# Performance work log

Measured on AMD Instinct MI355X. Metric: run time of the kernel, lower is better.

Reference implementation:

```python
import jax, jax.numpy as jnp
import numpy as np

N = 100000        # total nodes across the batch of graphs
E = 1600000       # directed edges (avg degree 16)
B = 64            # number of graphs
IN_C = 4
HID = 128


def gcn_conv(x, W, b, src, dst, n):
    """PyG GCNConv: add self-loops, symmetric deg normalization, scatter-add."""
    h = x @ W                                   # [n, out]
    loop = jnp.arange(n)
    s = jnp.concatenate([src, loop])            # [E+n] sources (with self-loops)
    d = jnp.concatenate([dst, loop])            # [E+n] targets
    deg = jax.ops.segment_sum(jnp.ones_like(s, dtype=h.dtype), d, num_segments=n)
    dinv = jnp.where(deg > 0, jax.lax.rsqrt(deg), 0.0)
    norm = dinv[s] * dinv[d]                    # [E+n]
    out = jax.ops.segment_sum(h[s] * norm[:, None], d, num_segments=n)
    return out + b


def setup_inputs() -> dict:
    key = jax.random.key(0)
    k1, k2, k3, k4, k5, k6, k7 = jax.random.split(key, 7)
    x = jax.random.normal(k1, (N, IN_C), dtype=jnp.float32)
    edge_index = jax.random.randint(k2, (2, E), 0, N, dtype=jnp.int64)
    batch = jnp.sort(jax.random.randint(k3, (N,), 0, B, dtype=jnp.int64))
    W1 = jax.random.normal(k4, (IN_C, HID), dtype=jnp.float32) / np.sqrt(IN_C)
    b1 = jnp.zeros((HID,), dtype=jnp.float32)
    W2 = jax.random.normal(k5, (HID, HID), dtype=jnp.float32) / np.sqrt(HID)
    b2 = jnp.zeros((HID,), dtype=jnp.float32)
    return {"x": x, "edge_index": edge_index, "batch": batch,
            "W1": W1, "b1": b1, "W2": W2, "b2": b2}


def reference(x, edge_index, batch, W1, b1, W2, b2):
    src, dst = edge_index[0], edge_index[1]
    n = x.shape[0]
    h = jax.nn.relu(gcn_conv(x, W1, b1, src, dst, n))
    h = jax.nn.relu(gcn_conv(h, W2, b2, src, dst, n))
    # global_mean_pool: scatter-mean by graph id
    s = jax.ops.segment_sum(h, batch, num_segments=B)                       # [B, HID]
    cnt = jax.ops.segment_sum(jnp.ones((n,), h.dtype), batch, num_segments=B)
    return s / jnp.maximum(cnt, 1.0)[:, None]
```

## Files before the change

### kernel.cpp

```cpp
#include <hip/hip_runtime.h>

#define TPB 256
#define HID 128
#define IN_C 4
#define SLOT_C 32
#define NB 512
#define EPT 8
#define ECAP 4096
#define OVF_CAP 131072

typedef __attribute__((ext_vector_type(8))) short bf16x8;
typedef __attribute__((ext_vector_type(4))) float f32x4;

union FragU { uint4 u; bf16x8 b; };

__device__ __forceinline__ unsigned f2bf(float f) {
    unsigned u = __float_as_uint(f);
    return (u + 0x7fffu + ((u >> 16) & 1u)) >> 16;
}
__device__ __forceinline__ float bf_lo(unsigned u) { return __uint_as_float(u << 16); }
__device__ __forceinline__ float bf_hi(unsigned u) { return __uint_as_float(u & 0xffff0000u); }

__global__ void k_prep(float* out, int n, int outsz,
                       const float* __restrict__ W2, unsigned short* w2f,
                       const int* __restrict__ batch, float* rcnt, int bg,
                       int* ovf_cnt, int* pcur) {
    int nbA = (n + TPB - 1) / TPB;
    int b = blockIdx.x;
    if (b < nbA) {
        int i = b * TPB + threadIdx.x;
        if (i < outsz) out[i] = 0.0f;
    } else if (b < nbA + 64) {
        int i = (b - nbA) * TPB + threadIdx.x;
        if (i < HID * HID) {
            int j = i & 7, frag = i >> 3;
            int lane = frag & 63, blk = frag >> 6;
            int kk = blk >> 3, nt = blk & 7;
            int quad = lane >> 4, nloc = lane & 15;
            int k = kk * 32 + quad * 8 + j;
            int c = nt * 16 + nloc;
            w2f[i] = (unsigned short)f2bf(W2[k * HID + c]);
        }
    } else {
        int g = threadIdx.x;
        if (g == 0) *ovf_cnt = 0;
        for (int z = g; z < NB; z += TPB) pcur[z] = 0;
        if (g < bg) {
            int lo0 = 0, hi0 = n;
            while (lo0 < hi0) { int m = (lo0 + hi0) >> 1; if (batch[m] < g) lo0 = m + 1; else hi0 = m; }
            int lo1 = lo0, hi1 = n;
            while (lo1 < hi1) { int m = (lo1 + hi1) >> 1; if (batch[m] < g + 1) lo1 = m + 1; else hi1 = m; }
            int c = lo1 - lo0;
            rcnt[g] = 1.0f / (float)(c > 1 ? c : 1);
        }
    }
}

__global__ __launch_bounds__(256) void k_part(
        const int* __restrict__ src, const int* __restrict__ dst,
        unsigned* elist, int* pcur, int e, int n) {
    __shared__ int lcnt[2][NB];
    __shared__ int lbase[NB];
    int t = threadIdx.x;
    int c = (t >> 5) & 1;
    for (int z = t; z < NB; z += 256) { lcnt[0][z] = 0; lcnt[1][z] = 0; }
    __syncthreads();

    int base_i = blockIdx.x * (256 * EPT);
    unsigned u[EPT]; int pr[EPT];
#pragma unroll
    for (int k = 0; k < EPT; k++) {
        int i = base_i + k * 256 + t;
        if (i < e) {
            int s = src[i];
            int d = dst[i];
            int p = (int)(((long long)d * NB) / n);
            int nlo = (int)(((long long)p * n + NB - 1) / NB);
            int r = atomicAdd(&lcnt[c][p], 1);
            pr[k] = p | (r << 9);
            u[k] = (unsigned)s | ((unsigned)(d - nlo) << 17);
        } else {
            pr[k] = -1;
        }
    }
    __syncthreads();

    for (int z = t; z < NB; z += 256) {
        int tot = lcnt[0][z] + lcnt[1][z];
        lbase[z] = tot ? atomicAdd(&pcur[z], tot) : 0;
    }
    __syncthreads();

#pragma unroll
    for (int k = 0; k < EPT; k++) {
        if (pr[k] >= 0) {
            int p = pr[k] & (NB - 1);
            int r = pr[k] >> 9;
            int idx = lbase[p] + (c ? lcnt[0][p] : 0) + r;
            if (idx < ECAP)
                elist[(size_t)p * ECAP + idx] = u[k];
        }
    }
}

__global__ __launch_bounds__(256) void k_build(
        const unsigned* __restrict__ elist, const int* __restrict__ pcur,
        int* cursor, float* dinv, int* slots, int* ovf, int* ovf_cnt, int n) {
    __shared__ int lcur[512];
    int p = blockIdx.x;
    int t = threadIdx.x;
    int nlo = (int)(((long long)p * n + NB - 1) / NB);
    int nhi = (int)(((long long)(p + 1) * n + NB - 1) / NB);
    int nn = nhi - nlo;
    for (int z = t; z < nn; z += 256) lcur[z] = 0;
    __syncthreads();

    int ne = pcur[p];
    if (ne > ECAP) ne = ECAP;
    for (int j = t; j < ne; j += 256) {
        unsigned u = elist[(size_t)p * ECAP + j];
        int s = (int)(u & 0x1FFFFu);
        int dloc = (int)(u >> 17);
        int pos = atomicAdd(&lcur[dloc], 1);
        if (pos < SLOT_C) {
            slots[(nlo + dloc) * SLOT_C + pos] = s;
        } else {
            int o = atomicAdd(ovf_cnt, 1);
            if (o < OVF_CAP) {
                ovf[2 * o] = s;
                ovf[2 * o + 1] = nlo + dloc;
            }
        }
    }
    __syncthreads();
    for (int z = t; z < nn; z += 256) {
        int dg = lcur[z];
        cursor[nlo + z] = dg;
        dinv[nlo + z] = rsqrtf((float)dg + 1.0f);
    }
}

__global__ __launch_bounds__(256) void k_g1f1(
        const int* __restrict__ cursor, const int* __restrict__ slots,
        const int* __restrict__ ovf, const int* __restrict__ ovf_cnt,
        const float* __restrict__ dinv, const float* __restrict__ x,
        const float* __restrict__ W1, const float* __restrict__ b1,
        unsigned* f1p, int n) {
    __shared__ float xs[256 * 5];
    int t = threadIdx.x;
    int v0 = blockIdx.x * 256;

    int v = v0 + t;
    if (v < n) {
        float dv = dinv[v];
        const float4* x4 = (const float4*)x;
        float4 xv = x4[v];
        float sl = dv * dv;
        float4 A = make_float4(sl * xv.x, sl * xv.y, sl * xv.z, sl * xv.w);
        float4 B = make_float4(0.f, 0.f, 0.f, 0.f);
        float4 C = make_float4(0.f, 0.f, 0.f, 0.f);
        float4 D = make_float4(0.f, 0.f, 0.f, 0.f);
        int deg = cursor[v];
        int m = deg < SLOT_C ? deg : SLOT_C;
        const int* sb = slots + v * SLOT_C;
        int e = 0;
        for (; e + 4 <= m; e += 4) {
            int s0 = sb[e], s1 = sb[e + 1], s2 = sb[e + 2], s3 = sb[e + 3];
            float n0 = dinv[s0] * dv, n1 = dinv[s1] * dv;
            float n2 = dinv[s2] * dv, n3 = dinv[s3] * dv;
            float4 r0 = x4[s0], r1 = x4[s1], r2 = x4[s2], r3 = x4[s3];
            A.x = fmaf(n0, r0.x, A.x); A.y = fmaf(n0, r0.y, A.y);
            A.z = fmaf(n0, r0.z, A.z); A.w = fmaf(n0, r0.w, A.w);
            B.x = fmaf(n1, r1.x, B.x); B.y = fmaf(n1, r1.y, B.y);
            B.z = fmaf(n1, r1.z, B.z); B.w = fmaf(n1, r1.w, B.w);
            C.x = fmaf(n2, r2.x, C.x); C.y = fmaf(n2, r2.y, C.y);
            C.z = fmaf(n2, r2.z, C.z); C.w = fmaf(n2, r2.w, C.w);
            D.x = fmaf(n3, r3.x, D.x); D.y = fmaf(n3, r3.y, D.y);
            D.z = fmaf(n3, r3.z, D.z); D.w = fmaf(n3, r3.w, D.w);
        }
        for (; e < m; e++) {
            int s = sb[e];
            float nm = dinv[s] * dv;
            float4 r = x4[s];
            A.x = fmaf(nm, r.x, A.x); A.y = fmaf(nm, r.y, A.y);
            A.z = fmaf(nm, r.z, A.z); A.w = fmaf(nm, r.w, A.w);
        }
        if (deg > SLOT_C) {
            int oc = *ovf_cnt;
            for (int k = 0; k < oc; k++) {
                if (ovf[2 * k + 1] == v) {
                    int s = ovf[2 * k];
                    float nm = dinv[s] * dv;
                    float4 r = x4[s];
                    A.x = fmaf(nm, r.x, A.x); A.y = fmaf(nm, r.y, A.y);
                    A.z = fmaf(nm, r.z, A.z); A.w = fmaf(nm, r.w, A.w);
                }
            }
        }
        xs[t * 5 + 0] = (A.x + B.x) + (C.x + D.x);
        xs[t * 5 + 1] = (A.y + B.y) + (C.y + D.y);
        xs[t * 5 + 2] = (A.z + B.z) + (C.z + D.z);
        xs[t * 5 + 3] = (A.w + B.w) + (C.w + D.w);
    }
    __syncthreads();

    int cp = t & 63;
    int c0 = cp * 2, c1 = c0 + 1;
    float w00 = W1[c0],           w01 = W1[c1];
    float w10 = W1[HID + c0],     w11 = W1[HID + c1];
    float w20 = W1[2 * HID + c0], w21 = W1[2 * HID + c1];
    float w30 = W1[3 * HID + c0], w31 = W1[3 * HID + c1];
    float bb0 = b1[c0],           bb1 = b1[c1];
    int g = t >> 6;
    for (int iter = 0; iter < 64; iter++) {
        int node = iter * 4 + g;
        int vv = v0 + node;
        if (vv >= n) break;
        float x0 = xs[node * 5 + 0], x1 = xs[node * 5 + 1];
        float x2 = xs[node * 5 + 2], x3 = xs[node * 5 + 3];
        float s0 = fmaf(x0, w00, fmaf(x1, w10, fmaf(x2, w20, fmaf(x3, w30, bb0))));
        float s1 = fmaf(x0, w01, fmaf(x1, w11, fmaf(x2, w21, fmaf(x3, w31, bb1))));
        s0 = s0 > 0.0f ? s0 : 0.0f;
        s1 = s1 > 0.0f ? s1 : 0.0f;
        f1p[(size_t)vv * 64 + cp] = f2bf(s0) | (f2bf(s1) << 16);
    }
}

__global__ __launch_bounds__(128) void k_gather2(
        const int* __restrict__ cursor, const int* __restrict__ slots,
        const int* __restrict__ ovf, const int* __restrict__ ovf_cnt,
        const float* __restrict__ dinv, const unsigned* __restrict__ f1p,
        unsigned* acc2b, int n) {
    int wv = threadIdx.x >> 6;
    int ln = threadIdx.x & 63;
    int h  = ln >> 5;
    int q  = ln & 31;
    int v = blockIdx.x * 2 + wv;
    if (v >= n) return;
    float dv = dinv[v];
    const uint2* F = (const uint2*)f1p;

    uint2 us = F[(size_t)v * 32 + q];
    float sl = (h == 0) ? dv * dv : 0.0f;
    float A[4] = { sl * bf_lo(us.x), sl * bf_hi(us.x),
                   sl * bf_lo(us.y), sl * bf_hi(us.y) };
    float B[4] = {0.f, 0.f, 0.f, 0.f};
    float C[4] = {0.f, 0.f, 0.f, 0.f};
    float D[4] = {0.f, 0.f, 0.f, 0.f};

    int deg = cursor[v];
    int m = deg < SLOT_C ? deg : SLOT_C;
    const int* sb = slots + v * SLOT_C;
    int e = 0;
    for (; e + 8 <= m; e += 8) {
        int sA = sb[e + h];
        int sB = sb[e + 2 + h];
        int sC = sb[e + 4 + h];
        int sD = sb[e + 6 + h];
        float nA = dinv[sA] * dv, nB = dinv[sB] * dv;
        float nC = dinv[sC] * dv, nD = dinv[sD] * dv;
        uint2 uA = F[(size_t)sA * 32 + q];
        uint2 uB = F[(size_t)sB * 32 + q];
        uint2 uC = F[(size_t)sC * 32 + q];
        uint2 uD = F[(size_t)sD * 32 + q];
        A[0] = fmaf(nA, bf_lo(uA.x), A[0]); A[1] = fmaf(nA, bf_hi(uA.x), A[1]);
        A[2] = fmaf(nA, bf_lo(uA.y), A[2]); A[3] = fmaf(nA, bf_hi(uA.y), A[3]);
        B[0] = fmaf(nB, bf_lo(uB.x), B[0]); B[1] = fmaf(nB, bf_hi(uB.x), B[1]);
        B[2] = fmaf(nB, bf_lo(uB.y), B[2]); B[3] = fmaf(nB, bf_hi(uB.y), B[3]);
        C[0] = fmaf(nC, bf_lo(uC.x), C[0]); C[1] = fmaf(nC, bf_hi(uC.x), C[1]);
        C[2] = fmaf(nC, bf_lo(uC.y), C[2]); C[3] = fmaf(nC, bf_hi(uC.y), C[3]);
        D[0] = fmaf(nD, bf_lo(uD.x), D[0]); D[1] = fmaf(nD, bf_hi(uD.x), D[1]);
        D[2] = fmaf(nD, bf_lo(uD.y), D[2]); D[3] = fmaf(nD, bf_hi(uD.y), D[3]);
    }
    for (; e + 2 <= m; e += 2) {
        int s = sb[e + h];
        float nm = dinv[s] * dv;
        uint2 u = F[(size_t)s * 32 + q];
        A[0] = fmaf(nm, bf_lo(u.x), A[0]); A[1] = fmaf(nm, bf_hi(u.x), A[1]);
        A[2] = fmaf(nm, bf_lo(u.y), A[2]); A[3] = fmaf(nm, bf_hi(u.y), A[3]);
    }
    if (e < m) {
        int s = sb[e];
        float nm = (h == 0) ? dinv[s] * dv : 0.0f;
        uint2 u = F[(size_t)s * 32 + q];
        A[0] = fmaf(nm, bf_lo(u.x), A[0]); A[1] = fmaf(nm, bf_hi(u.x), A[1]);
        A[2] = fmaf(nm, bf_lo(u.y), A[2]); A[3] = fmaf(nm, bf_hi(u.y), A[3]);
    }
    if (deg > SLOT_C) {
        int oc = *ovf_cnt;
        for (int k = 0; k < oc; k++) {
            if (ovf[2 * k + 1] == v && h == 0) {
                int s = ovf[2 * k];
                float nm = dinv[s] * dv;
                uint2 u = F[(size_t)s * 32 + q];
                A[0] = fmaf(nm, bf_lo(u.x), A[0]); A[1] = fmaf(nm, bf_hi(u.x), A[1]);
                A[2] = fmaf(nm, bf_lo(u.y), A[2]); A[3] = fmaf(nm, bf_hi(u.y), A[3]);
            }
        }
    }

    float o0 = (A[0] + B[0]) + (C[0] + D[0]);
    float o1 = (A[1] + B[1]) + (C[1] + D[1]);
    float o2 = (A[2] + B[2]) + (C[2] + D[2]);
    float o3 = (A[3] + B[3]) + (C[3] + D[3]);
    o0 += __shfl_xor(o0, 32, 64);
    o1 += __shfl_xor(o1, 32, 64);
    o2 += __shfl_xor(o2, 32, 64);
    o3 += __shfl_xor(o3, 32, 64);
    if (h == 0) {
        uint2 w;
        w.x = f2bf(o0) | (f2bf(o1) << 16);
        w.y = f2bf(o2) | (f2bf(o3) << 16);
        ((uint2*)acc2b)[(size_t)v * 32 + q] = w;
    }
}

__global__ __launch_bounds__(256) void k_mm2_pool(
        const unsigned* __restrict__ acc2b, const unsigned short* __restrict__ w2f,
        const float* __restrict__ b2, const int* __restrict__ batch,
        const float* __restrict__ rcnt, float* out, int n) {
    __shared__ int bch[64];
    int t = threadIdx.x;
    int w = t >> 6, lane = t & 63;
    int quad = lane >> 4, nloc = lane & 15;
    int v0 = blockIdx.x * 64;
    if (t < 64) {
        int v = v0 + t;
        bch[t] = (v < n) ? batch[v] : -1;
    }
    __syncthreads();

    int va = v0 + w * 16 + nloc;
    if (va >= n) va = n - 1;

    const uint4* A4 = (const uint4*)acc2b;
    const uint4* B4 = (const uint4*)w2f;

    f32x4 acc[8];
#pragma unroll
    for (int nt = 0; nt < 8; nt++) acc[nt] = (f32x4){0.f, 0.f, 0.f, 0.f};

#pragma unroll
    for (int kk = 0; kk < 4; kk++) {
        FragU af;
        af.u = A4[(size_t)va * 16 + kk * 4 + quad];
#pragma unroll
        for (int nt = 0; nt < 8; nt++) {
            FragU bf;
            bf.u = B4[(kk * 8 + nt) * 64 + lane];
            acc[nt] = __builtin_amdgcn_mfma_f32_16x16x32_bf16(af.b, bf.b, acc[nt], 0, 0, 0);
        }
    }

    int b0 = bch[w * 16], b15 = bch[w * 16 + 15];
    if (b0 == b15 && b0 >= 0) {
        float rc = rcnt[b0];
#pragma unroll
        for (int nt = 0; nt < 8; nt++) {
            float bias = b2[nt * 16 + nloc];
            float s = 0.f;
#pragma unroll
            for (int reg = 0; reg < 4; reg++) {
                float f = acc[nt][reg] + bias;
                s += f > 0.f ? f : 0.f;
            }
            s += __shfl_xor(s, 16, 64);
            s += __shfl_xor(s, 32, 64);
            if (lane < 16) atomicAdd(&out[b0 * HID + nt * 16 + lane], s * rc);
        }
    } else {
#pragma unroll
        for (int nt = 0; nt < 8; nt++) {
            float bias = b2[nt * 16 + nloc];
            int cur = -1; float run = 0.f;
#pragma unroll
            for (int reg = 0; reg < 4; reg++) {
                int b = bch[w * 16 + quad * 4 + reg];
                if (b < 0) continue;
                float f = acc[nt][reg] + bias;
                f = f > 0.f ? f : 0.f;
                if (b != cur) {
                    if (cur >= 0) atomicAdd(&out[cur * HID + nt * 16 + nloc], run * rcnt[cur]);
                    run = 0.f; cur = b;
                }
                run += f;
            }
            if (cur >= 0) atomicAdd(&out[cur * HID + nt * 16 + nloc], run * rcnt[cur]);
        }
    }
}

extern "C" void kernel_launch(void* const* d_in, const int* in_sizes, int n_in,
                              void* d_out, int out_size, void* d_ws, size_t ws_size,
                              hipStream_t stream) {
    const float* x   = (const float*)d_in[0];
    const int* ei    = (const int*)d_in[1];
    const int* batch = (const int*)d_in[2];
    const float* W1  = (const float*)d_in[3];
    const float* b1  = (const float*)d_in[4];
    const float* W2  = (const float*)d_in[5];
    const float* b2  = (const float*)d_in[6];
    float* out = (float*)d_out;

    int n  = in_sizes[0] / IN_C;
    int e  = in_sizes[1] / 2;
    int bg = out_size / HID;
    const int* src = ei;
    const int* dst = ei + e;

    size_t off_b = 0;
    char* base = (char*)d_ws;
    auto carve = [&](size_t bytes) -> void* {
        void* p = base + off_b;
        off_b += (bytes + 255) & ~(size_t)255;
        return p;
    };
    int*            cursor  = (int*)carve((size_t)n * 4);
    int*            slots   = (int*)carve((size_t)n * SLOT_C * 4);
    int*            ovf     = (int*)carve((size_t)OVF_CAP * 2 * 4);
    int*            ovf_cnt = (int*)carve(256);
    int*            pcur    = (int*)carve((size_t)NB * 4);
    unsigned*       elist   = (unsigned*)carve((size_t)NB * ECAP * 4);
    float*          dinv    = (float*)carve((size_t)n * 4);
    unsigned*       f1p     = (unsigned*)carve((size_t)n * 64 * 4);
    unsigned*       acc2b   = (unsigned*)carve((size_t)n * 64 * 4);
    unsigned short* w2f     = (unsigned short*)carve((size_t)HID * HID * 2);
    float*          rcnt    = (float*)carve((size_t)bg * 4);
    (void)ws_size;

    int gN = (n + TPB - 1) / TPB;
    int gP = (e + 256 * EPT - 1) / (256 * EPT);

    k_prep<<<gN + 64 + 1, TPB, 0, stream>>>(out, n, out_size, W2, w2f,
                                            batch, rcnt, bg, ovf_cnt, pcur);
    k_part<<<gP, TPB, 0, stream>>>(src, dst, elist, pcur, e, n);
    k_build<<<NB, TPB, 0, stream>>>(elist, pcur, cursor, dinv, slots, ovf, ovf_cnt, n);
    k_g1f1<<<gN, TPB, 0, stream>>>(cursor, slots, ovf, ovf_cnt, dinv, x, W1, b1, f1p, n);
    k_gather2<<<(n + 1) / 2, 128, 0, stream>>>(cursor, slots, ovf, ovf_cnt, dinv, f1p, acc2b, n);
    k_mm2_pool<<<(n + 63) / 64, 256, 0, stream>>>(acc2b, w2f, b2, batch, rcnt, out, n);
}
```

Before: 242.3 us.

## Fuse layer-2 gather with MFMA matmul and pooling via shared memory

Merges the second-layer neighbor gather and the W2 matmul plus mean-pool into one kernel. Each 1024-thread block gathers 16 node rows into shared memory, then 8 waves each compute one 16-column MFMA tile and do the pooled atomics. This removes the bf16 intermediate buffer round-trip through global memory and one kernel launch. In exchange, half the waves sit idle during the matmul phase, every block pays a barrier, and each block now issues more atomics to the output.

```diff
diff --git a/kernel.cpp b/kernel.cpp
--- a/kernel.cpp
+++ b/kernel.cpp
@@ -226,158 +226,137 @@
     }
 }
 
-__global__ __launch_bounds__(128) void k_gather2(
+__global__ __launch_bounds__(1024, 8) void k_g2mm(
         const int* __restrict__ cursor, const int* __restrict__ slots,
         const int* __restrict__ ovf, const int* __restrict__ ovf_cnt,
         const float* __restrict__ dinv, const unsigned* __restrict__ f1p,
-        unsigned* acc2b, int n) {
-    int wv = threadIdx.x >> 6;
-    int ln = threadIdx.x & 63;
-    int h  = ln >> 5;
-    int q  = ln & 31;
-    int v = blockIdx.x * 2 + wv;
-    if (v >= n) return;
-    float dv = dinv[v];
+        const unsigned short* __restrict__ w2f, const float* __restrict__ b2,
+        const int* __restrict__ batch, const float* __restrict__ rcnt,
+        float* out, int n) {
+    __shared__ unsigned arow[16][68];
+    __shared__ int bch[16];
+    int t = threadIdx.x;
+    int w = t >> 6, ln = t & 63;
+    int v0 = blockIdx.x * 16;
+    if (t < 16) bch[t] = (v0 + t < n) ? batch[v0 + t] : -1;
+
+    int h = ln >> 5;
+    int q = ln & 31;
+    int v = v0 + w;
     const uint2* F = (const uint2*)f1p;
-
-    uint2 us = F[(size_t)v * 32 + q];
-    float sl = (h == 0) ? dv * dv : 0.0f;
-    float A[4] = { sl * bf_lo(us.x), sl * bf_hi(us.x),
-                   sl * bf_lo(us.y), sl * bf_hi(us.y) };
-    float B[4] = {0.f, 0.f, 0.f, 0.f};
-    float C[4] = {0.f, 0.f, 0.f, 0.f};
-    float D[4] = {0.f, 0.f, 0.f, 0.f};
-
-    int deg = cursor[v];
-    int m = deg < SLOT_C ? deg : SLOT_C;
-    const int* sb = slots + v * SLOT_C;
-    int e = 0;
-    for (; e + 8 <= m; e += 8) {
-        int sA = sb[e + h];
-        int sB = sb[e + 2 + h];
-        int sC = sb[e + 4 + h];
-        int sD = sb[e + 6 + h];
-        float nA = dinv[sA] * dv, nB = dinv[sB] * dv;
-        float nC = dinv[sC] * dv, nD = dinv[sD] * dv;
-        uint2 uA = F[(size_t)sA * 32 + q];
-        uint2 uB = F[(size_t)sB * 32 + q];
-        uint2 uC = F[(size_t)sC * 32 + q];
-        uint2 uD = F[(size_t)sD * 32 + q];
-        A[0] = fmaf(nA, bf_lo(uA.x), A[0]); A[1] = fmaf(nA, bf_hi(uA.x), A[1]);
-        A[2] = fmaf(nA, bf_lo(uA.y), A[2]); A[3] = fmaf(nA, bf_hi(uA.y), A[3]);
-        B[0] = fmaf(nB, bf_lo(uB.x), B[0]); B[1] = fmaf(nB, bf_hi(uB.x), B[1]);
-        B[2] = fmaf(nB, bf_lo(uB.y), B[2]); B[3] = fmaf(nB, bf_hi(uB.y), B[3]);
-        C[0] = fmaf(nC, bf_lo(uC.x), C[0]); C[1] = fmaf(nC, bf_hi(uC.x), C[1]);
-        C[2] = fmaf(nC, bf_lo(uC.y), C[2]); C[3] = fmaf(nC, bf_hi(uC.y), C[3]);
-        D[0] = fmaf(nD, bf_lo(uD.x), D[0]); D[1] = fmaf(nD, bf_hi(uD.x), D[1]);
-        D[2] = fmaf(nD, bf_lo(uD.y), D[2]); D[3] = fmaf(nD, bf_hi(uD.y), D[3]);
-    }
-    for (; e + 2 <= m; e += 2) {
-        int s = sb[e + h];
-        float nm = dinv[s] * dv;
-        uint2 u = F[(size_t)s * 32 + q];
-        A[0] = fmaf(nm, bf_lo(u.x), A[0]); A[1] = fmaf(nm, bf_hi(u.x), A[1]);
-        A[2] = fmaf(nm, bf_lo(u.y), A[2]); A[3] = fmaf(nm, bf_hi(u.y), A[3]);
-    }
-    if (e < m) {
-        int s = sb[e];
-        float nm = (h == 0) ? dinv[s] * dv : 0.0f;
-        uint2 u = F[(size_t)s * 32 + q];
-        A[0] = fmaf(nm, bf_lo(u.x), A[0]); A[1] = fmaf(nm, bf_hi(u.x), A[1]);
-        A[2] = fmaf(nm, bf_lo(u.y), A[2]); A[3] = fmaf(nm, bf_hi(u.y), A[3]);
-    }
-    if (deg > SLOT_C) {
-        int oc = *ovf_cnt;
-        for (int k = 0; k < oc; k++) {
-            if (ovf[2 * k + 1] == v && h == 0) {
-                int s = ovf[2 * k];
-                float nm = dinv[s] * dv;
-                uint2 u = F[(size_t)s * 32 + q];
-                A[0] = fmaf(nm, bf_lo(u.x), A[0]); A[1] = fmaf(nm, bf_hi(u.x), A[1]);
-                A[2] = fmaf(nm, bf_lo(u.y), A[2]); A[3] = fmaf(nm, bf_hi(u.y), A[3]);
+    if (v < n) {
+        float dv = dinv[v];
+        uint2 us = F[(size_t)v * 32 + q];
+        float sl = (h == 0) ? dv * dv : 0.0f;
+        float A[4] = { sl * bf_lo(us.x), sl * bf_hi(us.x),
+                       sl * bf_lo(us.y), sl * bf_hi(us.y) };
+        float B[4] = {0.f, 0.f, 0.f, 0.f};
+        float C[4] = {0.f, 0.f, 0.f, 0.f};
+        float D[4] = {0.f, 0.f, 0.f, 0.f};
+
+        int deg = cursor[v];
+        int m = deg < SLOT_C ? deg : SLOT_C;
+        const int* sb = slots + v * SLOT_C;
+        int e = 0;
+        for (; e + 8 <= m; e += 8) {
+            int sA = sb[e + h];
+            int sB = sb[e + 2 + h];
+            int sC = sb[e + 4 + h];
+            int sD = sb[e + 6 + h];
+            float nA = dinv[sA] * dv, nB = dinv[sB] * dv;
+            float nC = dinv[sC] * dv, nD = dinv[sD] * dv;
+            uint2 uA = F[(size_t)sA * 32 + q];
+            uint2 uB = F[(size_t)sB * 32 + q];
+            uint2 uC = F[(size_t)sC * 32 + q];
+            uint2 uD = F[(size_t)sD * 32 + q];
+            A[0] = fmaf(nA, bf_lo(uA.x), A[0]); A[1] = fmaf(nA, bf_hi(uA.x), A[1]);
+            A[2] = fmaf(nA, bf_lo(uA.y), A[2]); A[3] = fmaf(nA, bf_hi(uA.y), A[3]);
+            B[0] = fmaf(nB, bf_lo(uB.x), B[0]); B[1] = fmaf(nB, bf_hi(uB.x), B[1]);
+            B[2] = fmaf(nB, bf_lo(uB.y), B[2]); B[3] = fmaf(nB, bf_hi(uB.y), B[3]);
+            C[0] = fmaf(nC, bf_lo(uC.x), C[0]); C[1] = fmaf(nC, bf_hi(uC.x), C[1]);
+            C[2] = fmaf(nC, bf_lo(uC.y), C[2]); C[3] = fmaf(nC, bf_hi(uC.y), C[3]);
+            D[0] = fmaf(nD, bf_lo(uD.x), D[0]); D[1] = fmaf(nD, bf_hi(uD.x), D[1]);
+            D[2] = fmaf(nD, bf_lo(uD.y), D[2]); D[3] = fmaf(nD, bf_hi(uD.y), D[3]);
+        }
+        for (; e + 2 <= m; e += 2) {
+            int s = sb[e + h];
+            float nm = dinv[s] * dv;
+            uint2 u = F[(size_t)s * 32 + q];
+            A[0] = fmaf(nm, bf_lo(u.x), A[0]); A[1] = fmaf(nm, bf_hi(u.x), A[1]);
+            A[2] = fmaf(nm, bf_lo(u.y), A[2]); A[3] = fmaf(nm, bf_hi(u.y), A[3]);
+        }
+        if (e < m) {
+            int s = sb[e];
+            float nm = (h == 0) ? dinv[s] * dv : 0.0f;
+            uint2 u = F[(size_t)s * 32 + q];
+            A[0] = fmaf(nm, bf_lo(u.x), A[0]); A[1] = fmaf(nm, bf_hi(u.x), A[1]);
+            A[2] = fmaf(nm, bf_lo(u.y), A[2]); A[3] = fmaf(nm, bf_hi(u.y), A[3]);
+        }
+        if (deg > SLOT_C) {
+            int oc = *ovf_cnt;
+            for (int k = 0; k < oc; k++) {
+                if (ovf[2 * k + 1] == v && h == 0) {
+                    int s = ovf[2 * k];
+                    float nm = dinv[s] * dv;
+                    uint2 u = F[(size_t)s * 32 + q];
+                    A[0] = fmaf(nm, bf_lo(u.x), A[0]); A[1] = fmaf(nm, bf_hi(u.x), A[1]);
+                    A[2] = fmaf(nm, bf_lo(u.y), A[2]); A[3] = fmaf(nm, bf_hi(u.y), A[3]);
+                }
             }
         }
-    }
-
-    float o0 = (A[0] + B[0]) + (C[0] + D[0]);
-    float o1 = (A[1] + B[1]) + (C[1] + D[1]);
-    float o2 = (A[2] + B[2]) + (C[2] + D[2]);
-    float o3 = (A[3] + B[3]) + (C[3] + D[3]);
-    o0 += __shfl_xor(o0, 32, 64);
-    o1 += __shfl_xor(o1, 32, 64);
-    o2 += __shfl_xor(o2, 32, 64);
-    o3 += __shfl_xor(o3, 32, 64);
-    if (h == 0) {
-        uint2 w;
-        w.x = f2bf(o0) | (f2bf(o1) << 16);
-        w.y = f2bf(o2) | (f2bf(o3) << 16);
-        ((uint2*)acc2b)[(size_t)v * 32 + q] = w;
-    }
-}
-
-__global__ __launch_bounds__(256) void k_mm2_pool(
-        const unsigned* __restrict__ acc2b, const unsigned short* __restrict__ w2f,
-        const float* __restrict__ b2, const int* __restrict__ batch,
-        const float* __restrict__ rcnt, float* out, int n) {
-    __shared__ int bch[64];
-    int t = threadIdx.x;
-    int w = t >> 6, lane = t & 63;
-    int quad = lane >> 4, nloc = lane & 15;
-    int v0 = blockIdx.x * 64;
-    if (t < 64) {
-        int v = v0 + t;
-        bch[t] = (v < n) ? batch[v] : -1;
-    }
-    __syncthreads();
-
-    int va = v0 + w * 16 + nloc;
-    if (va >= n) va = n - 1;
-
-    const uint4* A4 = (const uint4*)acc2b;
-    const uint4* B4 = (const uint4*)w2f;
-
-    f32x4 acc[8];
+
+        float o0 = (A[0] + B[0]) + (C[0] + D[0]);
+        float o1 = (A[1] + B[1]) + (C[1] + D[1]);
+        float o2 = (A[2] + B[2]) + (C[2] + D[2]);
+        float o3 = (A[3] + B[3]) + (C[3] + D[3]);
+        o0 += __shfl_xor(o0, 32, 64);
+        o1 += __shfl_xor(o1, 32, 64);
+        o2 += __shfl_xor(o2, 32, 64);
+        o3 += __shfl_xor(o3, 32, 64);
+        if (h == 0) {
+            arow[w][2 * q]     = f2bf(o0) | (f2bf(o1) << 16);
+            arow[w][2 * q + 1] = f2bf(o2) | (f2bf(o3) << 16);
+        }
+    } else {
+        if (h == 0) { arow[w][2 * q] = 0; arow[w][2 * q + 1] = 0; }
+    }
+    __syncthreads();
+
+    if (w < 8) {
+        int nt = w;
+        int lane = ln;
+        int quad = lane >> 4, nloc = lane & 15;
+        const uint4* B4 = (const uint4*)w2f;
+
+        f32x4 acc = (f32x4){0.f, 0.f, 0.f, 0.f};
 #pragma unroll
-    for (int nt = 0; nt < 8; nt++) acc[nt] = (f32x4){0.f, 0.f, 0.f, 0.f};
-
-#pragma unroll
-    for (int kk = 0; kk < 4; kk++) {
-        FragU af;
-        af.u = A4[(size_t)va * 16 + kk * 4 + quad];
-#pragma unroll
-        for (int nt = 0; nt < 8; nt++) {
-            FragU bf;
+        for (int kk = 0; kk < 4; kk++) {
+            FragU af, bf;
+            af.u = *(const uint4*)&arow[nloc][(kk * 4 + quad) * 4];
             bf.u = B4[(kk * 8 + nt) * 64 + lane];
-            acc[nt] = __builtin_amdgcn_mfma_f32_16x16x32_bf16(af.b, bf.b, acc[nt], 0, 0, 0);
-        }
-    }
-
-    int b0 = bch[w * 16], b15 = bch[w * 16 + 15];
-    if (b0 == b15 && b0 >= 0) {
-        float rc = rcnt[b0];
-#pragma unroll
-        for (int nt = 0; nt < 8; nt++) {
-            float bias = b2[nt * 16 + nloc];
+            acc = __builtin_amdgcn_mfma_f32_16x16x32_bf16(af.b, bf.b, acc, 0, 0, 0);
+        }
+
+        int b0 = bch[0], b15 = bch[15];
+        float bias = b2[nt * 16 + nloc];
+        if (b0 == b15 && b0 >= 0) {
+            float rc = rcnt[b0];
             float s = 0.f;
 #pragma unroll
             for (int reg = 0; reg < 4; reg++) {
-                float f = acc[nt][reg] + bias;
+                float f = acc[reg] + bias;
                 s += f > 0.f ? f : 0.f;
             }
             s += __shfl_xor(s, 16, 64);
             s += __shfl_xor(s, 32, 64);
             if (lane < 16) atomicAdd(&out[b0 * HID + nt * 16 + lane], s * rc);
-        }
-    } else {
-#pragma unroll
-        for (int nt = 0; nt < 8; nt++) {
-            float bias = b2[nt * 16 + nloc];
+        } else {
             int cur = -1; float run = 0.f;
 #pragma unroll
             for (int reg = 0; reg < 4; reg++) {
-                int b = bch[w * 16 + quad * 4 + reg];
+                int b = bch[quad * 4 + reg];
                 if (b < 0) continue;
-                float f = acc[nt][reg] + bias;
+                float f = acc[reg] + bias;
                 f = f > 0.f ? f : 0.f;
                 if (b != cur) {
                     if (cur >= 0) atomicAdd(&out[cur * HID + nt * 16 + nloc], run * rcnt[cur]);
@@ -423,7 +402,6 @@
     unsigned*       elist   = (unsigned*)carve((size_t)NB * ECAP * 4);
     float*          dinv    = (float*)carve((size_t)n * 4);
     unsigned*       f1p     = (unsigned*)carve((size_t)n * 64 * 4);
-    unsigned*       acc2b   = (unsigned*)carve((size_t)n * 64 * 4);
     unsigned short* w2f     = (unsigned short*)carve((size_t)HID * HID * 2);
     float*          rcnt    = (float*)carve((size_t)bg * 4);
     (void)ws_size;
@@ -436,6 +414,6 @@
     k_part<<<gP, TPB, 0, stream>>>(src, dst, elist, pcur, e, n);
     k_build<<<NB, TPB, 0, stream>>>(elist, pcur, cursor, dinv, slots, ovf, ovf_cnt, n);
     k_g1f1<<<gN, TPB, 0, stream>>>(cursor, slots, ovf, ovf_cnt, dinv, x, W1, b1, f1p, n);
-    k_gather2<<<(n + 1) / 2, 128, 0, stream>>>(cursor, slots, ovf, ovf_cnt, dinv, f1p, acc2b, n);
-    k_mm2_pool<<<(n + 63) / 64, 256, 0, stream>>>(acc2b, w2f, b2, batch, rcnt, out, n);
-}
+    k_g2mm<<<(n + 15) / 16, 1024, 0, stream>>>(cursor, slots, ovf, ovf_cnt, dinv, f1p,
+                                               w2f, b2, batch, rcnt, out, n);
+}
```

Measured after the change: 242.1 us. About the same (-0.1%).

## Apply W2 before aggregation and fuse bias, relu and mean pooling into gather

Applied to the files above, without the earlier changes.

Reorders layer two to compute H·W2 first with MFMA into a bf16 table, then aggregates neighbours of the transformed features, and applies bias, ReLU and mean-pool atomics inside the gather kernel. This removes the separate post-aggregation matmul-pool pass and its per-node staging before pooling. In exchange, every node now does 128 fp32 atomicAdds into only 64 graph rows, which can bring heavy atomic contention, and rounding changes slightly because W2 is applied before the sum.

```diff
diff --git a/kernel.cpp b/kernel.cpp
--- a/kernel.cpp
+++ b/kernel.cpp
@@ -226,11 +226,54 @@
     }
 }
 
-__global__ __launch_bounds__(128) void k_gather2(
+__global__ __launch_bounds__(256) void k_hw2(
+        const unsigned* __restrict__ f1p, const unsigned short* __restrict__ w2f,
+        unsigned* gtab, int n) {
+    int t = threadIdx.x;
+    int w = t >> 6, lane = t & 63;
+    int quad = lane >> 4, nloc = lane & 15;
+    int v0 = blockIdx.x * 64;
+    int va = v0 + w * 16 + nloc;
+    int vc = va < n ? va : n - 1;
+    const uint4* A4 = (const uint4*)f1p;
+    const uint4* B4 = (const uint4*)w2f;
+
+    f32x4 acc[8];
+#pragma unroll
+    for (int nt = 0; nt < 8; nt++) acc[nt] = (f32x4){0.f, 0.f, 0.f, 0.f};
+
+#pragma unroll
+    for (int kk = 0; kk < 4; kk++) {
+        FragU af;
+        af.u = A4[(size_t)vc * 16 + kk * 4 + quad];
+#pragma unroll
+        for (int nt = 0; nt < 8; nt++) {
+            FragU bf;
+            bf.u = B4[(kk * 8 + nt) * 64 + lane];
+            acc[nt] = __builtin_amdgcn_mfma_f32_16x16x32_bf16(af.b, bf.b, acc[nt], 0, 0, 0);
+        }
+    }
+
+    int rbase = v0 + w * 16 + quad * 4;
+#pragma unroll
+    for (int nt = 0; nt < 8; nt++) {
+#pragma unroll
+        for (int reg = 0; reg < 4; reg++) {
+            unsigned bv = f2bf(acc[nt][reg]);
+            unsigned hv = (unsigned)__shfl_xor((int)bv, 1, 64);
+            int r = rbase + reg;
+            if (!(nloc & 1) && r < n)
+                gtab[(size_t)r * 64 + nt * 8 + (nloc >> 1)] = bv | (hv << 16);
+        }
+    }
+}
+
+__global__ __launch_bounds__(128) void k_gpool(
         const int* __restrict__ cursor, const int* __restrict__ slots,
         const int* __restrict__ ovf, const int* __restrict__ ovf_cnt,
-        const float* __restrict__ dinv, const unsigned* __restrict__ f1p,
-        unsigned* acc2b, int n) {
+        const float* __restrict__ dinv, const unsigned* __restrict__ gtab,
+        const float* __restrict__ b2, const int* __restrict__ batch,
+        const float* __restrict__ rcnt, float* out, int n) {
     int wv = threadIdx.x >> 6;
     int ln = threadIdx.x & 63;
     int h  = ln >> 5;
@@ -238,7 +281,7 @@
     int v = blockIdx.x * 2 + wv;
     if (v >= n) return;
     float dv = dinv[v];
-    const uint2* F = (const uint2*)f1p;
+    const uint2* F = (const uint2*)gtab;
 
     uint2 us = F[(size_t)v * 32 + q];
     float sl = (h == 0) ? dv * dv : 0.0f;
@@ -308,85 +351,18 @@
     o2 += __shfl_xor(o2, 32, 64);
     o3 += __shfl_xor(o3, 32, 64);
     if (h == 0) {
-        uint2 w;
-        w.x = f2bf(o0) | (f2bf(o1) << 16);
-        w.y = f2bf(o2) | (f2bf(o3) << 16);
-        ((uint2*)acc2b)[(size_t)v * 32 + q] = w;
-    }
-}
-
-__global__ __launch_bounds__(256) void k_mm2_pool(
-        const unsigned* __restrict__ acc2b, const unsigned short* __restrict__ w2f,
-        const float* __restrict__ b2, const int* __restrict__ batch,
-        const float* __restrict__ rcnt, float* out, int n) {
-    __shared__ int bch[64];
-    int t = threadIdx.x;
-    int w = t >> 6, lane = t & 63;
-    int quad = lane >> 4, nloc = lane & 15;
-    int v0 = blockIdx.x * 64;
-    if (t < 64) {
-        int v = v0 + t;
-        bch[t] = (v < n) ? batch[v] : -1;
-    }
-    __syncthreads();
-
-    int va = v0 + w * 16 + nloc;
-    if (va >= n) va = n - 1;
-
-    const uint4* A4 = (const uint4*)acc2b;
-    const uint4* B4 = (const uint4*)w2f;
-
-    f32x4 acc[8];
-#pragma unroll
-    for (int nt = 0; nt < 8; nt++) acc[nt] = (f32x4){0.f, 0.f, 0.f, 0.f};
-
-#pragma unroll
-    for (int kk = 0; kk < 4; kk++) {
-        FragU af;
-        af.u = A4[(size_t)va * 16 + kk * 4 + quad];
-#pragma unroll
-        for (int nt = 0; nt < 8; nt++) {
-            FragU bf;
-            bf.u = B4[(kk * 8 + nt) * 64 + lane];
-            acc[nt] = __builtin_amdgcn_mfma_f32_16x16x32_bf16(af.b, bf.b, acc[nt], 0, 0, 0);
-        }
-    }
-
-    int b0 = bch[w * 16], b15 = bch[w * 16 + 15];
-    if (b0 == b15 && b0 >= 0) {
-        float rc = rcnt[b0];
-#pragma unroll
-        for (int nt = 0; nt < 8; nt++) {
-            float bias = b2[nt * 16 + nloc];
-            float s = 0.f;
-#pragma unroll
-            for (int reg = 0; reg < 4; reg++) {
-                float f = acc[nt][reg] + bias;
-                s += f > 0.f ? f : 0.f;
-            }
-            s += __shfl_xor(s, 16, 64);
-            s += __shfl_xor(s, 32, 64);
-            if (lane < 16) atomicAdd(&out[b0 * HID + nt * 16 + lane], s * rc);
-        }
-    } else {
-#pragma unroll
-        for (int nt = 0; nt < 8; nt++) {
-            float bias = b2[nt * 16 + nloc];
-            int cur = -1; float run = 0.f;
-#pragma unroll
-            for (int reg = 0; reg < 4; reg++) {
-                int b = bch[w * 16 + quad * 4 + reg];
-                if (b < 0) continue;
-                float f = acc[nt][reg] + bias;
-                f = f > 0.f ? f : 0.f;
-                if (b != cur) {
-                    if (cur >= 0) atomicAdd(&out[cur * HID + nt * 16 + nloc], run * rcnt[cur]);
-                    run = 0.f; cur = b;
-                }
-                run += f;
-            }
-            if (cur >= 0) atomicAdd(&out[cur * HID + nt * 16 + nloc], run * rcnt[cur]);
-        }
+        int b = batch[v];
+        float rc = rcnt[b];
+        float4 bb = ((const float4*)b2)[q];
+        float r0 = o0 + bb.x; r0 = r0 > 0.f ? r0 : 0.f;
+        float r1 = o1 + bb.y; r1 = r1 > 0.f ? r1 : 0.f;
+        float r2 = o2 + bb.z; r2 = r2 > 0.f ? r2 : 0.f;
+        float r3 = o3 + bb.w; r3 = r3 > 0.f ? r3 : 0.f;
+        float* orow = out + (size_t)b * HID + 4 * q;
+        atomicAdd(orow + 0, r0 * rc);
+        atomicAdd(orow + 1, r1 * rc);
+        atomicAdd(orow + 2, r2 * rc);
+        atomicAdd(orow + 3, r3 * rc);
     }
 }
 
@@ -423,7 +399,7 @@
     unsigned*       elist   = (unsigned*)carve((size_t)NB * ECAP * 4);
     float*          dinv    = (float*)carve((size_t)n * 4);
     unsigned*       f1p     = (unsigned*)carve((size_t)n * 64 * 4);
-    unsigned*       acc2b   = (unsigned*)carve((size_t)n * 64 * 4);
+    unsigned*       gtab    = (unsigned*)carve((size_t)n * 64 * 4);
     unsigned short* w2f     = (unsigned short*)carve((size_t)HID * HID * 2);
     float*          rcnt    = (float*)carve((size_t)bg * 4);
     (void)ws_size;
@@ -436,6 +412,7 @@
     k_part<<<gP, TPB, 0, stream>>>(src, dst, elist, pcur, e, n);
     k_build<<<NB, TPB, 0, stream>>>(elist, pcur, cursor, dinv, slots, ovf, ovf_cnt, n);
     k_g1f1<<<gN, TPB, 0, stream>>>(cursor, slots, ovf, ovf_cnt, dinv, x, W1, b1, f1p, n);
-    k_gather2<<<(n + 1) / 2, 128, 0, stream>>>(cursor, slots, ovf, ovf_cnt, dinv, f1p, acc2b, n);
-    k_mm2_pool<<<(n + 63) / 64, 256, 0, stream>>>(acc2b, w2f, b2, batch, rcnt, out, n);
-}
+    k_hw2<<<(n + 63) / 64, 256, 0, stream>>>(f1p, w2f, gtab, n);
+    k_gpool<<<(n + 1) / 2, 128, 0, stream>>>(cursor, slots, ovf, ovf_cnt, dinv, gtab,
+                                             b2, batch, rcnt, out, n);
+}
```

Result: slower. 920.2 us (+279.7%).
